# Performance work log

Hardware: AMD Instinct MI355X
Metric: run time of the kernel (lower is better)

## Reference

```python
import jax, jax.numpy as jnp
import numpy as np

HEADS, DIM_HEAD = 8, 96
DIM = HEADS * DIM_HEAD            # 768
DEPTH = 8
MEM_LAYERS = (4, 5)               # layers with KNN-retrieval attention
TOPK = 32                         # num_retrieved_memories
CLIP_LEN, PREFIX_LEN = 10, 10
NEG = -1e9


def layernorm(x, g, b):
    m = x.mean(-1, keepdims=True)
    v = ((x - m) ** 2).mean(-1, keepdims=True)
    return (x - m) * jax.lax.rsqrt(v + 1e-5) * g + b


def attention(x, wq_l, wkv_l, wo_l, mem_k=None, mem_v=None):
    # one-headed key/values (memorizing-transformers style), multi-head queries
    b, n, _ = x.shape
    q = (x @ wq_l).reshape(b, n, HEADS, DIM_HEAD).transpose(0, 2, 1, 3)  # [b,h,n,d]
    q = q * (DIM_HEAD ** -0.5)
    kv = x @ wkv_l                                   # [b,n,2d]
    k, v = kv[..., :DIM_HEAD], kv[..., DIM_HEAD:]    # [b,n,d] each
    sim = jnp.einsum('bhid,bjd->bhij', q, k)         # local scores
    causal = jnp.tril(jnp.ones((n, n), dtype=bool))
    sim = jnp.where(causal, sim, NEG)
    if mem_k is not None:
        # exact inner-product top-k retrieval from per-batch memory bank
        mem_sim = jnp.einsum('bhid,bmd->bhim', q, mem_k)      # [b,h,n,M]
        top_sim, top_idx = jax.lax.top_k(mem_sim, TOPK)       # [b,h,n,K]
        mem_v_sel = jnp.take_along_axis(
            mem_v[:, None, None], top_idx[..., None], axis=3)  # [b,h,n,K,d]
        attn = jax.nn.softmax(jnp.concatenate([top_sim, sim], axis=-1), axis=-1)
        mem_attn, loc_attn = attn[..., :TOPK], attn[..., TOPK:]
        out = (jnp.einsum('bhij,bhijd->bhid', mem_attn, mem_v_sel)
               + jnp.einsum('bhij,bjd->bhid', loc_attn, v))
    else:
        attn = jax.nn.softmax(sim, axis=-1)
        out = jnp.einsum('bhij,bjd->bhid', attn, v)
    out = out.transpose(0, 2, 1, 3).reshape(b, n, DIM)
    return out @ wo_l


def setup_inputs() -> dict:
    key = jax.random.key(0)
    ks = jax.random.split(key, 12)
    s = 0.02
    inp = {
        'x': jax.random.normal(ks[0], (16, 640), jnp.float32),
        'linear_w': jax.random.normal(ks[1], (640, CLIP_LEN * DIM), jnp.float32) * s,
        'linear_b': jnp.zeros((CLIP_LEN * DIM,), jnp.float32),
        'prefix_const': jax.random.normal(ks[2], (PREFIX_LEN, DIM), jnp.float32),
        'ln1_g': jnp.ones((DEPTH, DIM), jnp.float32),
        'ln1_b': jnp.zeros((DEPTH, DIM), jnp.float32),
        'wq': jax.random.normal(ks[3], (DEPTH, DIM, DIM), jnp.float32) * s,
        'wkv': jax.random.normal(ks[4], (DEPTH, DIM, 2 * DIM_HEAD), jnp.float32) * s,
        'wo': jax.random.normal(ks[5], (DEPTH, DIM, DIM), jnp.float32) * s,
        'ln2_g': jnp.ones((DEPTH, DIM), jnp.float32),
        'ln2_b': jnp.zeros((DEPTH, DIM), jnp.float32),
        'w1': jax.random.normal(ks[6], (DEPTH, DIM, 4 * DIM), jnp.float32) * s,
        'b1': jnp.zeros((DEPTH, 4 * DIM), jnp.float32),
        'w2': jax.random.normal(ks[7], (DEPTH, 4 * DIM, DIM), jnp.float32) * s,
        'b2': jnp.zeros((DEPTH, DIM), jnp.float32),
        'lnf_g': jnp.ones((DIM,), jnp.float32),
        'lnf_b': jnp.zeros((DIM,), jnp.float32),
        'mem_k': jax.random.normal(ks[8], (16, 32768, DIM_HEAD), jnp.float32),
        'mem_v': jax.random.normal(ks[9], (16, 32768, DIM_HEAD), jnp.float32),
    }
    return inp


def reference(x, linear_w, linear_b, prefix_const,
              ln1_g, ln1_b, wq, wkv, wo, ln2_g, ln2_b,
              w1, b1, w2, b2, lnf_g, lnf_b, mem_k, mem_v):
    b = x.shape[0]
    # linear projection of clip feature -> clip_length tokens
    h = (x @ linear_w + linear_b).reshape(b, CLIP_LEN, DIM)
    prefix = jnp.broadcast_to(prefix_const[None], (b, PREFIX_LEN, DIM))
    t = jnp.concatenate([h, prefix], axis=1)  # [b, 20, dim]
    for l in range(DEPTH):
        mk, mv = (mem_k, mem_v) if l in MEM_LAYERS else (None, None)
        t = t + attention(layernorm(t, ln1_g[l], ln1_b[l]), wq[l], wkv[l], wo[l], mk, mv)
        hf = layernorm(t, ln2_g[l], ln2_b[l])
        t = t + (jax.nn.gelu(hf @ w1[l] + b1[l]) @ w2[l] + b2[l])
    t = layernorm(t, lnf_g, lnf_b)
    return t[:, CLIP_LEN:]  # [b, prefix_length, dim]
```

## Files before the change

### kernel.cpp

```cpp
#include <hip/hip_runtime.h>
#include <hip/hip_bf16.h>

#define BB 16
#define NSEQ 20
#define HEADS 8
#define DH 96
#define DIM 768
#define FF 3072
#define KMEM 32768
#define NCHUNK 4
#define CHUNK 8192
#define CAP 128

typedef unsigned short u16;
typedef __attribute__((ext_vector_type(8))) short short8v;
typedef __attribute__((ext_vector_type(4))) float f32x4;

__device__ __forceinline__ u16 f2bu(float x) {
    __hip_bfloat16 h = __float2bfloat16(x);
    return *reinterpret_cast<u16*>(&h);
}

__global__ __launch_bounds__(256) void conv_k(const float* __restrict__ src, u16* __restrict__ dst, int n)
{
    int i = blockIdx.x * 256 + threadIdx.x;
    if (i < n) dst[i] = f2bu(src[i]);
}

__device__ __forceinline__ void tconv_tile(const float* __restrict__ src, u16* __restrict__ dst,
                                           int K, int N, int kt, int nt, int tx, int ty)
{
    __shared__ float tile[32][33];
    int k0 = kt * 32, n0 = nt * 32;
#pragma unroll
    for (int i = 0; i < 4; i++)
        tile[ty + 8 * i][tx] = src[(size_t)(k0 + ty + 8 * i) * N + n0 + tx];
    __syncthreads();
#pragma unroll
    for (int i = 0; i < 4; i++)
        dst[(size_t)(n0 + ty + 8 * i) * K + k0 + tx] = f2bu(tile[tx][ty + 8 * i]);
}

__global__ __launch_bounds__(256) void tconv_k(const float* __restrict__ src, u16* __restrict__ dst, int K, int N)
{
    int tilesN = N >> 5;
    tconv_tile(src, dst, K, N, blockIdx.x / tilesN, blockIdx.x % tilesN,
               threadIdx.x & 31, threadIdx.x >> 5);
}

__global__ __launch_bounds__(256) void wconv5L_k(const float* __restrict__ wq, const float* __restrict__ wkv,
    const float* __restrict__ wo, const float* __restrict__ w1, const float* __restrict__ w2,
    u16* __restrict__ wt, size_t wtStride)
{
    int l = blockIdx.y;
    wq += (size_t)l * 589824;
    wkv += (size_t)l * 147456;
    wo += (size_t)l * 589824;
    w1 += (size_t)l * 2359296;
    w2 += (size_t)l * 2359296;
    wt += (size_t)l * wtStride;
    int bx = blockIdx.x;
    int tx = threadIdx.x & 31, ty = threadIdx.x >> 5;
    if (bx < 576)       tconv_tile(wq,  wt + 0,       768, 768,  bx / 24,          bx % 24,          tx, ty);
    else if (bx < 720)  tconv_tile(wkv, wt + 589824,  768, 192,  (bx - 576) / 6,   (bx - 576) % 6,   tx, ty);
    else if (bx < 1296) tconv_tile(wo,  wt + 737280,  768, 768,  (bx - 720) / 24,  (bx - 720) % 24,  tx, ty);
    else if (bx < 3600) tconv_tile(w1,  wt + 1327104, 768, 3072, (bx - 1296) / 96, (bx - 1296) % 96, tx, ty);
    else                tconv_tile(w2,  wt + 3686400, 3072, 768, (bx - 3600) / 24, (bx - 3600) % 24, tx, ty);
}

__device__ __forceinline__ void storeC(float* C, size_t idx, float v) { C[idx] = v; }
__device__ __forceinline__ void storeC(u16* C, size_t idx, float v)   { C[idx] = f2bu(v); }

template <typename CT>
__global__ __launch_bounds__(256) void gemm_bt(const u16* __restrict__ A, const u16* __restrict__ Bt,
    const float* __restrict__ bias, const float* __restrict__ resid, CT* __restrict__ C,
    int M, int N, int K, int lda, int ldc, float scale, int act)
{
    int tid = threadIdx.x;
    int w = tid >> 6, lane = tid & 63;
    int m0 = blockIdx.y * 16;
    int n0 = blockIdx.x * 128 + w * 32;
    int row = lane & 15;
    int kg  = lane >> 4;
    const u16* arow = A + (size_t)(m0 + row) * lda + kg * 8;
    int c0 = n0 + row;
    int c1 = n0 + 16 + row;
    const u16* bt0 = Bt + (size_t)min(c0, N - 1) * K + kg * 8;
    const u16* bt1 = Bt + (size_t)min(c1, N - 1) * K + kg * 8;
    f32x4 acc0 = {0.f, 0.f, 0.f, 0.f};
    f32x4 acc1 = {0.f, 0.f, 0.f, 0.f};
#pragma unroll 4
    for (int k0 = 0; k0 < K; k0 += 32) {
        short8v af = *(const short8v*)(arow + k0);
        short8v b0 = *(const short8v*)(bt0 + k0);
        short8v b1 = *(const short8v*)(bt1 + k0);
        acc0 = __builtin_amdgcn_mfma_f32_16x16x32_bf16(af, b0, acc0, 0, 0, 0);
        acc1 = __builtin_amdgcn_mfma_f32_16x16x32_bf16(af, b1, acc1, 0, 0, 0);
    }
#pragma unroll
    for (int r = 0; r < 4; r++) {
        int rw = m0 + kg * 4 + r;
        if (c0 < N) {
            float v = acc0[r] * scale;
            if (bias) v += bias[c0];
            if (act) {
                float xx = v;
                float tt = 0.7978845608028654f * (xx + 0.044715f * xx * xx * xx);
                v = 0.5f * xx * (1.0f + tanhf(tt));
            }
            if (resid) v += resid[(size_t)rw * ldc + c0];
            storeC(C, (size_t)rw * ldc + c0, v);
        }
        if (c1 < N) {
            float v = acc1[r] * scale;
            if (bias) v += bias[c1];
            if (act) {
                float xx = v;
                float tt = 0.7978845608028654f * (xx + 0.044715f * xx * xx * xx);
                v = 0.5f * xx * (1.0f + tanhf(tt));
            }
            if (resid) v += resid[(size_t)rw * ldc + c1];
            storeC(C, (size_t)rw * ldc + c1, v);
        }
    }
}

__global__ __launch_bounds__(256) void gemm_qkv(const u16* __restrict__ A, const u16* __restrict__ Bt,
    float* __restrict__ qb, float* __restrict__ kvb, float qscale)
{
    const int N = 960, K = DIM;
    int tid = threadIdx.x;
    int w = tid >> 6, lane = tid & 63;
    int m0 = blockIdx.y * 16;
    int n0 = blockIdx.x * 128 + w * 32;
    int row = lane & 15;
    int kg  = lane >> 4;
    const u16* arow = A + (size_t)(m0 + row) * K + kg * 8;
    int c0 = n0 + row;
    int c1 = n0 + 16 + row;
    const u16* bt0 = Bt + (size_t)min(c0, N - 1) * K + kg * 8;
    const u16* bt1 = Bt + (size_t)min(c1, N - 1) * K + kg * 8;
    f32x4 acc0 = {0.f, 0.f, 0.f, 0.f};
    f32x4 acc1 = {0.f, 0.f, 0.f, 0.f};
#pragma unroll 4
    for (int k0 = 0; k0 < K; k0 += 32) {
        short8v af = *(const short8v*)(arow + k0);
        short8v b0 = *(const short8v*)(bt0 + k0);
        short8v b1 = *(const short8v*)(bt1 + k0);
        acc0 = __builtin_amdgcn_mfma_f32_16x16x32_bf16(af, b0, acc0, 0, 0, 0);
        acc1 = __builtin_amdgcn_mfma_f32_16x16x32_bf16(af, b1, acc1, 0, 0, 0);
    }
#pragma unroll
    for (int r = 0; r < 4; r++) {
        int rw = m0 + kg * 4 + r;
        if (c0 < 768)      qb[(size_t)rw * 768 + c0] = acc0[r] * qscale;
        else if (c0 < 960) kvb[(size_t)rw * 192 + (c0 - 768)] = acc0[r];
        if (c1 < 768)      qb[(size_t)rw * 768 + c1] = acc1[r] * qscale;
        else if (c1 < 960) kvb[(size_t)rw * 192 + (c1 - 768)] = acc1[r];
    }
}

__global__ __launch_bounds__(256) void ln_k(const float* __restrict__ x, const float* __restrict__ g,
    const float* __restrict__ bb, u16* __restrict__ y)
{
    int row = blockIdx.x;
    const float* xr = x + (size_t)row * DIM;
    int tid = threadIdx.x;
    float v0 = xr[tid], v1 = xr[tid + 256], v2 = xr[tid + 512];
    __shared__ float red[4];
    float s = v0 + v1 + v2;
    for (int off = 32; off; off >>= 1) s += __shfl_down(s, off);
    if ((tid & 63) == 0) red[tid >> 6] = s;
    __syncthreads();
    float mean = (red[0] + red[1] + red[2] + red[3]) * (1.f / 768.f);
    __syncthreads();
    float d0 = v0 - mean, d1 = v1 - mean, d2 = v2 - mean;
    s = d0 * d0 + d1 * d1 + d2 * d2;
    for (int off = 32; off; off >>= 1) s += __shfl_down(s, off);
    if ((tid & 63) == 0) red[tid >> 6] = s;
    __syncthreads();
    float var = (red[0] + red[1] + red[2] + red[3]) * (1.f / 768.f);
    float rs = rsqrtf(var + 1e-5f);
    u16* yr = y + (size_t)row * DIM;
    yr[tid]       = f2bu(d0 * rs * g[tid]       + bb[tid]);
    yr[tid + 256] = f2bu(d1 * rs * g[tid + 256] + bb[tid + 256]);
    yr[tid + 512] = f2bu(d2 * rs * g[tid + 512] + bb[tid + 512]);
}

__global__ __launch_bounds__(256) void lnf_k(const float* __restrict__ x, const float* __restrict__ g,
    const float* __restrict__ bb, float* __restrict__ out)
{
    int blk = blockIdx.x;
    int b = blk / 10, ii = blk - b * 10;
    int row = b * NSEQ + 10 + ii;
    const float* xr = x + (size_t)row * DIM;
    int tid = threadIdx.x;
    float v0 = xr[tid], v1 = xr[tid + 256], v2 = xr[tid + 512];
    __shared__ float red[4];
    float s = v0 + v1 + v2;
    for (int off = 32; off; off >>= 1) s += __shfl_down(s, off);
    if ((tid & 63) == 0) red[tid >> 6] = s;
    __syncthreads();
    float mean = (red[0] + red[1] + red[2] + red[3]) * (1.f / 768.f);
    __syncthreads();
    float d0 = v0 - mean, d1 = v1 - mean, d2 = v2 - mean;
    s = d0 * d0 + d1 * d1 + d2 * d2;
    for (int off = 32; off; off >>= 1) s += __shfl_down(s, off);
    if ((tid & 63) == 0) red[tid >> 6] = s;
    __syncthreads();
    float var = (red[0] + red[1] + red[2] + red[3]) * (1.f / 768.f);
    float rs = rsqrtf(var + 1e-5f);
    float* orow = out + ((size_t)(b * 10 + ii)) * DIM;
    orow[tid]       = d0 * rs * g[tid]       + bb[tid];
    orow[tid + 256] = d1 * rs * g[tid + 256] + bb[tid + 256];
    orow[tid + 512] = d2 * rs * g[tid + 512] + bb[tid + 512];
}

__global__ __launch_bounds__(256) void prefix_k(const float* __restrict__ p, float* __restrict__ t)
{
    int idx = blockIdx.x * 256 + threadIdx.x;
    if (idx < BB * 7680) {
        int b = idx / 7680;
        int r = idx - b * 7680;
        t[(size_t)b * (NSEQ * DIM) + 7680 + r] = p[r];
    }
}

__device__ __forceinline__ float dot96(const float* __restrict__ a, const float* __restrict__ b)
{
    float s = 0.f;
#pragma unroll
    for (int d4 = 0; d4 < 24; d4++) {
        float4 av = *(const float4*)(a + d4 * 4);
        float4 bv = *(const float4*)(b + d4 * 4);
        s = fmaf(av.x, bv.x, s);
        s = fmaf(av.y, bv.y, s);
        s = fmaf(av.z, bv.z, s);
        s = fmaf(av.w, bv.w, s);
    }
    return s;
}

__global__ __launch_bounds__(256) void lattn_k(const float* __restrict__ q, const float* __restrict__ kv,
    u16* __restrict__ ao)
{
    int b = blockIdx.x, h = blockIdx.y;
    __shared__ float sims[NSEQ][NSEQ];
    __shared__ float probs[NSEQ][NSEQ];
    const float* qb = q + (size_t)b * NSEQ * DIM + h * DH;
    const float* kb = kv + (size_t)b * NSEQ * 192;
    int tid = threadIdx.x;
    for (int p = tid; p < NSEQ * NSEQ; p += 256) {
        int i = p / NSEQ, j = p - i * NSEQ;
        float s;
        if (j > i) s = -1.0e9f;
        else s = dot96(qb + (size_t)i * DIM, kb + j * 192);
        sims[i][j] = s;
    }
    __syncthreads();
    if (tid < NSEQ) {
        int i = tid;
        float m = -1e30f;
        for (int j = 0; j < NSEQ; j++) m = fmaxf(m, sims[i][j]);
        float sum = 0.f;
        for (int j = 0; j < NSEQ; j++) { float e = expf(sims[i][j] - m); probs[i][j] = e; sum += e; }
        float inv = 1.f / sum;
        for (int j = 0; j < NSEQ; j++) probs[i][j] *= inv;
    }
    __syncthreads();
    for (int p = tid; p < NSEQ * DH; p += 256) {
        int i = p / DH, d = p - i * DH;
        float o = 0.f;
        for (int j = 0; j <= i; j++) o = fmaf(probs[i][j], kb[j * 192 + 96 + d], o);
        ao[((size_t)b * NSEQ + i) * DIM + h * DH + d] = f2bu(o);
    }
}

__device__ __forceinline__ bool tk_better(float va, int ia, float vb, int ib) {
    return (va > vb) || (va == vb && ia < ib);
}

__device__ __forceinline__ void lds_fence() {
    asm volatile("s_waitcnt lgkmcnt(0)" ::: "memory");
    __builtin_amdgcn_sched_barrier(0);
}

__device__ void topk32(float* bv, int* bi, int cnt, int lane,
                       float& ov, int& oi, float& thr_out) {
    lds_fence();
    float v0 = (lane < cnt)      ? bv[lane]      : -3.0e38f;
    int   i0 = (lane < cnt)      ? bi[lane]      : 0x7fffffff;
    float v1 = (lane + 64 < cnt) ? bv[lane + 64] : -3.0e38f;
    int   i1 = (lane + 64 < cnt) ? bi[lane + 64] : 0x7fffffff;
    lds_fence();
#pragma unroll
    for (int k = 2; k <= 128; k <<= 1) {
#pragma unroll
        for (int j = 64; j >= 1; j >>= 1) {
            if (j >= k) continue;
            if (j == 64) {
                bool asc = ((lane & k) == 0);
                bool b01 = tk_better(v0, i0, v1, i1);
                if (b01 != asc) { float tv = v0; int ti = i0; v0 = v1; i0 = i1; v1 = tv; i1 = ti; }
            } else {
                {
                    float pv = __shfl_xor(v0, j); int pi = __shfl_xor(i0, j);
                    bool asc = ((lane & k) == 0);
                    bool first = ((lane & j) == 0);
                    bool mb = tk_better(v0, i0, pv, pi);
                    bool keep = first ? (mb == asc) : (mb != asc);
                    if (!keep) { v0 = pv; i0 = pi; }
                }
                {
                    float pv = __shfl_xor(v1, j); int pi = __shfl_xor(i1, j);
                    bool asc = (((lane + 64) & k) == 0);
                    bool first = ((lane & j) == 0);
                    bool mb = tk_better(v1, i1, pv, pi);
                    bool keep = first ? (mb == asc) : (mb != asc);
                    if (!keep) { v1 = pv; i1 = pi; }
                }
            }
        }
    }
    if (lane < 32) { bv[lane] = v0; bi[lane] = i0; }
    lds_fence();
    ov = v0; oi = i0;
    thr_out = __shfl(v0, 31);
}

__device__ __forceinline__ void tk_pass(const float4 kr[6], const float4 qreg[5][6],
    float thrR[5], int cntR[5], float (*bufv)[CAP], int (*bufi)[CAP],
    int r0, int lane, int qt, int key)
{
    float a[5];
#pragma unroll
    for (int rr = 0; rr < 5; rr++) a[rr] = 0.f;
#pragma unroll
    for (int i = 0; i < 6; i++) {
        float4 kv = kr[i];
#pragma unroll
        for (int rr = 0; rr < 5; rr++) {
            float4 qv = qreg[rr][i];
            a[rr] = fmaf(qv.x, kv.x, a[rr]);
            a[rr] = fmaf(qv.y, kv.y, a[rr]);
            a[rr] = fmaf(qv.z, kv.z, a[rr]);
            a[rr] = fmaf(qv.w, kv.w, a[rr]);
        }
    }
#pragma unroll
    for (int rr = 0; rr < 5; rr++) {
        a[rr] += __shfl_xor(a[rr], 1);
        a[rr] += __shfl_xor(a[rr], 2);
    }
#pragma unroll
    for (int rr = 0; rr < 5; rr++) {
        bool cand = (qt == 0) && (a[rr] >= thrR[rr]);
        unsigned long long mask = __ballot(cand);
        int n = __popcll(mask);
        if (n) {
            int r = r0 + rr;
            if (cntR[rr] + n > CAP) {
                float dv; int di;
                topk32(&bufv[r][0], &bufi[r][0], cntR[rr], lane, dv, di, thrR[rr]);
                cntR[rr] = 32;
            }
            int pos = cntR[rr] + __popcll(mask & ((1ull << lane) - 1ull));
            if (cand) { bufv[r][pos] = a[rr]; bufi[r][pos] = key; }
            cntR[rr] += n;
        }
    }
}

__global__ __launch_bounds__(256) __attribute__((amdgpu_waves_per_eu(2, 2)))
void memtopk_k(const float* __restrict__ q, const float* __restrict__ memk,
    float* __restrict__ tkv, int* __restrict__ tki)
{
    __shared__ float bufv[NSEQ][CAP];
    __shared__ int   bufi[NSEQ][CAP];
    int c = blockIdx.x, h = blockIdx.y, b = blockIdx.z;
    int tid = threadIdx.x;
    int lane = tid & 63;
    int w = tid >> 6;
    int r0 = w * 5;
    int qt = lane & 3;
    int kk = lane >> 2;

    float4 qreg[5][6];
#pragma unroll
    for (int rr = 0; rr < 5; rr++) {
        const float4* qrow = (const float4*)(q + ((size_t)(b * NSEQ + r0 + rr)) * DIM + h * DH + qt * 24);
#pragma unroll
        for (int i = 0; i < 6; i++) qreg[rr][i] = qrow[i];
    }

    float thrR[5]; int cntR[5];
#pragma unroll
    for (int rr = 0; rr < 5; rr++) { thrR[rr] = -3.0e38f; cntR[rr] = 0; }

    const float* kbase = memk + (size_t)b * KMEM * DH;
    int k0 = c * CHUNK;

    float4 kA[12], kB[12];
#pragma unroll
    for (int s = 0; s < 2; s++) {
        const float4* kp = (const float4*)(kbase + (size_t)(k0 + s * 16 + kk) * DH + qt * 24);
#pragma unroll
        for (int i = 0; i < 6; i++) kA[s * 6 + i] = kp[i];
    }
    for (int p = 0; p < CHUNK / 16; p += 4) {
        int key0 = k0 + p * 16 + kk;
#pragma unroll
        for (int s = 0; s < 2; s++) {
            const float4* kp = (const float4*)(kbase + (size_t)(key0 + (32 + s * 16)) * DH + qt * 24);
#pragma unroll
            for (int i = 0; i < 6; i++) kB[s * 6 + i] = kp[i];
        }
        tk_pass(kA + 0, qreg, thrR, cntR, bufv, bufi, r0, lane, qt, key0);
        tk_pass(kA + 6, qreg, thrR, cntR, bufv, bufi, r0, lane, qt, key0 + 16);
        if (p + 4 < CHUNK / 16) {
#pragma unroll
            for (int s = 0; s < 2; s++) {
                const float4* kp = (const float4*)(kbase + (size_t)(key0 + (64 + s * 16)) * DH + qt * 24);
#pragma unroll
                for (int i = 0; i < 6; i++) kA[s * 6 + i] = kp[i];
            }
        }
        tk_pass(kB + 0, qreg, thrR, cntR, bufv, bufi, r0, lane, qt, key0 + 32);
        tk_pass(kB + 6, qreg, thrR, cntR, bufv, bufi, r0, lane, qt, key0 + 48);
    }
#pragma unroll
    for (int rr = 0; rr < 5; rr++) {
        int r = r0 + rr;
        float ov; int oi; float dthr;
        topk32(&bufv[r][0], &bufi[r][0], cntR[rr], lane, ov, oi, dthr);
        if (lane < 32) {
            size_t base = ((((size_t)b * HEADS + h) * NSEQ + r) * NCHUNK + c) * 32;
            tkv[base + lane] = ov;
            tki[base + lane] = oi;
        }
    }
}

__global__ __launch_bounds__(64) void memattn_k(const float* __restrict__ q, const float* __restrict__ kv,
    const float* __restrict__ memv, const float* __restrict__ tkv, const int* __restrict__ tki,
    u16* __restrict__ ao)
{
    int i = blockIdx.x, h = blockIdx.y, b = blockIdx.z;
    __shared__ float cv[NCHUNK * 32];
    __shared__ int   ci[NCHUNK * 32];
    __shared__ float selv[32];
    __shared__ int   seli[32];
    __shared__ float ls[NSEQ];
    __shared__ float probs[52];
    int tid = threadIdx.x;
    size_t base = (((size_t)b * HEADS + h) * NSEQ + i) * (NCHUNK * 32);
#pragma unroll
    for (int s = 0; s < NCHUNK * 32 / 64; s++) {
        cv[tid + 64 * s] = tkv[base + tid + 64 * s];
        ci[tid + 64 * s] = tki[base + tid + 64 * s];
    }
    const float* qr = q + ((size_t)b * NSEQ + i) * DIM + h * DH;
    const float* kvb = kv + (size_t)b * NSEQ * 192;
    if (tid <= i) {
        float s = dot96(qr, kvb + tid * 192);
        ls[tid] = s;
    }
    __syncthreads();
    for (int r = 0; r < 32; r++) {
        float bv = -3.0e38f; int bidx = 0x7fffffff; int bs = 0;
#pragma unroll
        for (int s = 0; s < NCHUNK * 32 / 64; s++) {
            float v = cv[tid + 64 * s]; int ix = ci[tid + 64 * s];
            if (tk_better(v, ix, bv, bidx)) { bv = v; bidx = ix; bs = tid + 64 * s; }
        }
        for (int off = 32; off; off >>= 1) {
            float ovv = __shfl_down(bv, off);
            int oii = __shfl_down(bidx, off);
            int oss = __shfl_down(bs, off);
            if (tk_better(ovv, oii, bv, bidx)) { bv = ovv; bidx = oii; bs = oss; }
        }
        if (tid == 0) { selv[r] = bv; seli[r] = bidx; cv[bs] = -3.0e38f; }
        __syncthreads();
    }
    if (tid == 0) {
        float m = -1e30f;
        for (int r = 0; r < 32; r++) m = fmaxf(m, selv[r]);
        for (int j = 0; j <= i; j++) m = fmaxf(m, ls[j]);
        float sum = 0.f;
        for (int r = 0; r < 32; r++) { float e = expf(selv[r] - m); probs[r] = e; sum += e; }
        for (int j = 0; j <= i; j++) { float e = expf(ls[j] - m); probs[32 + j] = e; sum += e; }
        float inv = 1.f / sum;
        for (int r = 0; r < 32 + i + 1; r++) probs[r] *= inv;
    }
    __syncthreads();
    const float* mvb = memv + (size_t)b * KMEM * DH;
    for (int d = tid; d < DH; d += 64) {
        float o = 0.f;
        for (int r = 0; r < 32; r++) o = fmaf(probs[r], mvb[(size_t)seli[r] * DH + d], o);
        for (int j = 0; j <= i; j++) o = fmaf(probs[32 + j], kvb[j * 192 + 96 + d], o);
        ao[((size_t)b * NSEQ + i) * DIM + h * DH + d] = f2bu(o);
    }
}

extern "C" void kernel_launch(void* const* d_in, const int* in_sizes, int n_in,
                              void* d_out, int out_size, void* d_ws, size_t ws_size,
                              hipStream_t stream) {
    const float* x            = (const float*)d_in[0];
    const float* linear_w     = (const float*)d_in[1];
    const float* linear_b     = (const float*)d_in[2];
    const float* prefix_const = (const float*)d_in[3];
    const float* ln1_g        = (const float*)d_in[4];
    const float* ln1_b        = (const float*)d_in[5];
    const float* wq           = (const float*)d_in[6];
    const float* wkv          = (const float*)d_in[7];
    const float* wo           = (const float*)d_in[8];
    const float* ln2_g        = (const float*)d_in[9];
    const float* ln2_b        = (const float*)d_in[10];
    const float* w1           = (const float*)d_in[11];
    const float* b1           = (const float*)d_in[12];
    const float* w2           = (const float*)d_in[13];
    const float* b2           = (const float*)d_in[14];
    const float* lnf_g        = (const float*)d_in[15];
    const float* lnf_b        = (const float*)d_in[16];
    const float* mem_k        = (const float*)d_in[17];
    const float* mem_v        = (const float*)d_in[18];

    float* ws = (float*)d_ws;
    float* t    = ws;
    u16*   yb   = (u16*)(ws + 245760);
    float* qb   = ws + 491520;
    float* kvb  = ws + 737280;
    u16*   aob  = (u16*)(ws + 798720);
    u16*   h1b  = (u16*)(ws + 1044480);
    float* tkv  = ws + 2027520;
    int*   tki  = (int*)(ws + 2355200);
    u16*   wt   = (u16*)(ws + 2682880);
    float* out  = (float*)d_out;

    const size_t LAYER_WT = 6045696;
    const int all8 = (ws_size >= (size_t)(2682880 + 8 * 3022848 + 2560) * 4) ? 1 : 0;
    u16* xb = (u16*)(ws + (all8 ? (2682880 + 8 * 3022848) : (2682880 + 3022848)));

    const float qscale = 0.10206207261596577f;
    const size_t WOT = 737280, W1T = 1327104, W2T = 3686400;

    conv_k<<<40, 256, 0, stream>>>(x, xb, 16 * 640);
    tconv_k<<<4800, 256, 0, stream>>>(linear_w, wt, 640, 7680);
    gemm_bt<float><<<dim3(60, 1), 256, 0, stream>>>(xb, wt, linear_b, nullptr, t,
                                                    16, 7680, 640, 640, 15360, 1.f, 0);
    prefix_k<<<dim3(480), 256, 0, stream>>>(prefix_const, t);

    if (all8)
        wconv5L_k<<<dim3(5904, 8), 256, 0, stream>>>(wq, wkv, wo, w1, w2, wt, LAYER_WT);

    for (int l = 0; l < 8; l++) {
        u16* wtl = wt + (all8 ? (size_t)l * LAYER_WT : 0);
        if (!all8)
            wconv5L_k<<<dim3(5904, 1), 256, 0, stream>>>(wq + (size_t)l * 589824, wkv + (size_t)l * 147456,
                                                         wo + (size_t)l * 589824, w1 + (size_t)l * 2359296,
                                                         w2 + (size_t)l * 2359296, wtl, 0);
        ln_k<<<320, 256, 0, stream>>>(t, ln1_g + (size_t)l * DIM, ln1_b + (size_t)l * DIM, yb);
        gemm_qkv<<<dim3(8, 20), 256, 0, stream>>>(yb, wtl, qb, kvb, qscale);
        if (l == 4 || l == 5) {
            memtopk_k<<<dim3(NCHUNK, HEADS, BB), 256, 0, stream>>>(qb, mem_k, tkv, tki);
            memattn_k<<<dim3(NSEQ, HEADS, BB), 64, 0, stream>>>(qb, kvb, mem_v, tkv, tki, aob);
        } else {
            lattn_k<<<dim3(BB, HEADS), 256, 0, stream>>>(qb, kvb, aob);
        }
        gemm_bt<float><<<dim3(6, 20), 256, 0, stream>>>(aob, wtl + WOT, nullptr, t, t,
                                                        320, 768, 768, 768, 768, 1.f, 0);
        ln_k<<<320, 256, 0, stream>>>(t, ln2_g + (size_t)l * DIM, ln2_b + (size_t)l * DIM, yb);
        gemm_bt<u16><<<dim3(24, 20), 256, 0, stream>>>(yb, wtl + W1T, b1 + (size_t)l * FF, nullptr, h1b,
                                                       320, 3072, 768, 768, 3072, 1.f, 1);
        gemm_bt<float><<<dim3(6, 20), 256, 0, stream>>>(h1b, wtl + W2T, b2 + (size_t)l * DIM, t, t,
                                                        320, 768, 3072, 3072, 768, 1.f, 0);
    }
    lnf_k<<<160, 256, 0, stream>>>(t, lnf_g, lnf_b, out);
}
```

Measured before the change: 2.078 ms.

## Fuse layernorm into QKV and FFN-up GEMMs, batch ballots in top-k scan

Removes the standalone layernorm kernels. The QKV and W1 GEMMs now each normalize their 16-row A tile into shared memory before running the MFMA loop, which saves 16 launches and the bf16 round trip through global memory. The cost is that every column block recomputes the layernorm for its rows (8x or 24x redundant work). The memory top-k scan also gathers all five row ballots first and skips the insertion path when none are set, to cut divergent branching in the hot loop.

```diff
diff --git a/kernel.cpp b/kernel.cpp
--- a/kernel.cpp
+++ b/kernel.cpp
@@ -11,6 +11,7 @@
 #define NCHUNK 4
 #define CHUNK 8192
 #define CAP 128
+#define ALDS 776
 
 typedef unsigned short u16;
 typedef __attribute__((ext_vector_type(8))) short short8v;
@@ -125,17 +126,63 @@
     }
 }
 
-__global__ __launch_bounds__(256) void gemm_qkv(const u16* __restrict__ A, const u16* __restrict__ Bt,
+__device__ __forceinline__ void ln_stage(const float* __restrict__ t, const float* __restrict__ g,
+    const float* __restrict__ bln, int m0, int tid, u16* __restrict__ As)
+{
+    int lane = tid & 63, w = tid >> 6;
+    int rl = w * 4 + (lane >> 4);
+    int sl = lane & 15;
+    const float4* tr = (const float4*)(t + (size_t)(m0 + rl) * DIM);
+    float4 xv[12];
+    float sum = 0.f;
+#pragma unroll
+    for (int i = 0; i < 12; i++) {
+        xv[i] = tr[i * 16 + sl];
+        sum += xv[i].x + xv[i].y + xv[i].z + xv[i].w;
+    }
+    sum += __shfl_xor(sum, 1); sum += __shfl_xor(sum, 2);
+    sum += __shfl_xor(sum, 4); sum += __shfl_xor(sum, 8);
+    float mean = sum * (1.f / 768.f);
+    float vs = 0.f;
+#pragma unroll
+    for (int i = 0; i < 12; i++) {
+        float dx = xv[i].x - mean, dy = xv[i].y - mean;
+        float dz = xv[i].z - mean, dw2 = xv[i].w - mean;
+        vs += dx * dx + dy * dy + dz * dz + dw2 * dw2;
+    }
+    vs += __shfl_xor(vs, 1); vs += __shfl_xor(vs, 2);
+    vs += __shfl_xor(vs, 4); vs += __shfl_xor(vs, 8);
+    float rs = rsqrtf(vs * (1.f / 768.f) + 1e-5f);
+    u16* arow = As + (size_t)rl * ALDS;
+#pragma unroll
+    for (int i = 0; i < 12; i++) {
+        int col = i * 64 + sl * 4;
+        float4 gv = *(const float4*)(g + col);
+        float4 bv = *(const float4*)(bln + col);
+        ushort4 ov;
+        ov.x = f2bu((xv[i].x - mean) * rs * gv.x + bv.x);
+        ov.y = f2bu((xv[i].y - mean) * rs * gv.y + bv.y);
+        ov.z = f2bu((xv[i].z - mean) * rs * gv.z + bv.z);
+        ov.w = f2bu((xv[i].w - mean) * rs * gv.w + bv.w);
+        *(ushort4*)(arow + col) = ov;
+    }
+}
+
+__global__ __launch_bounds__(256) void gemm_ln_qkv(const float* __restrict__ t,
+    const float* __restrict__ g, const float* __restrict__ bln, const u16* __restrict__ Bt,
     float* __restrict__ qb, float* __restrict__ kvb, float qscale)
 {
+    __shared__ u16 As[16 * ALDS];
     const int N = 960, K = DIM;
     int tid = threadIdx.x;
+    int m0 = blockIdx.y * 16;
+    ln_stage(t, g, bln, m0, tid, As);
+    __syncthreads();
     int w = tid >> 6, lane = tid & 63;
-    int m0 = blockIdx.y * 16;
     int n0 = blockIdx.x * 128 + w * 32;
     int row = lane & 15;
     int kg  = lane >> 4;
-    const u16* arow = A + (size_t)(m0 + row) * K + kg * 8;
+    const u16* arow = As + (size_t)row * ALDS + kg * 8;
     int c0 = n0 + row;
     int c1 = n0 + 16 + row;
     const u16* bt0 = Bt + (size_t)min(c0, N - 1) * K + kg * 8;
@@ -160,31 +207,51 @@
     }
 }
 
-__global__ __launch_bounds__(256) void ln_k(const float* __restrict__ x, const float* __restrict__ g,
-    const float* __restrict__ bb, u16* __restrict__ y)
-{
-    int row = blockIdx.x;
-    const float* xr = x + (size_t)row * DIM;
+__global__ __launch_bounds__(256) void gemm_ln_w1(const float* __restrict__ t,
+    const float* __restrict__ g, const float* __restrict__ bln, const u16* __restrict__ Bt,
+    const float* __restrict__ bias, u16* __restrict__ C)
+{
+    __shared__ u16 As[16 * ALDS];
+    const int N = FF, K = DIM;
     int tid = threadIdx.x;
-    float v0 = xr[tid], v1 = xr[tid + 256], v2 = xr[tid + 512];
-    __shared__ float red[4];
-    float s = v0 + v1 + v2;
-    for (int off = 32; off; off >>= 1) s += __shfl_down(s, off);
-    if ((tid & 63) == 0) red[tid >> 6] = s;
-    __syncthreads();
-    float mean = (red[0] + red[1] + red[2] + red[3]) * (1.f / 768.f);
-    __syncthreads();
-    float d0 = v0 - mean, d1 = v1 - mean, d2 = v2 - mean;
-    s = d0 * d0 + d1 * d1 + d2 * d2;
-    for (int off = 32; off; off >>= 1) s += __shfl_down(s, off);
-    if ((tid & 63) == 0) red[tid >> 6] = s;
-    __syncthreads();
-    float var = (red[0] + red[1] + red[2] + red[3]) * (1.f / 768.f);
-    float rs = rsqrtf(var + 1e-5f);
-    u16* yr = y + (size_t)row * DIM;
-    yr[tid]       = f2bu(d0 * rs * g[tid]       + bb[tid]);
-    yr[tid + 256] = f2bu(d1 * rs * g[tid + 256] + bb[tid + 256]);
-    yr[tid + 512] = f2bu(d2 * rs * g[tid + 512] + bb[tid + 512]);
+    int m0 = blockIdx.y * 16;
+    ln_stage(t, g, bln, m0, tid, As);
+    __syncthreads();
+    int w = tid >> 6, lane = tid & 63;
+    int n0 = blockIdx.x * 128 + w * 32;
+    int row = lane & 15;
+    int kg  = lane >> 4;
+    const u16* arow = As + (size_t)row * ALDS + kg * 8;
+    int c0 = n0 + row;
+    int c1 = n0 + 16 + row;
+    const u16* bt0 = Bt + (size_t)c0 * K + kg * 8;
+    const u16* bt1 = Bt + (size_t)c1 * K + kg * 8;
+    f32x4 acc0 = {0.f, 0.f, 0.f, 0.f};
+    f32x4 acc1 = {0.f, 0.f, 0.f, 0.f};
+#pragma unroll 4
+    for (int k0 = 0; k0 < K; k0 += 32) {
+        short8v af = *(const short8v*)(arow + k0);
+        short8v b0 = *(const short8v*)(bt0 + k0);
+        short8v b1 = *(const short8v*)(bt1 + k0);
+        acc0 = __builtin_amdgcn_mfma_f32_16x16x32_bf16(af, b0, acc0, 0, 0, 0);
+        acc1 = __builtin_amdgcn_mfma_f32_16x16x32_bf16(af, b1, acc1, 0, 0, 0);
+    }
+#pragma unroll
+    for (int r = 0; r < 4; r++) {
+        int rw = m0 + kg * 4 + r;
+        {
+            float v = acc0[r] + bias[c0];
+            float tt = 0.7978845608028654f * (v + 0.044715f * v * v * v);
+            v = 0.5f * v * (1.0f + tanhf(tt));
+            C[(size_t)rw * FF + c0] = f2bu(v);
+        }
+        {
+            float v = acc1[r] + bias[c1];
+            float tt = 0.7978845608028654f * (v + 0.044715f * v * v * v);
+            v = 0.5f * v * (1.0f + tanhf(tt));
+            C[(size_t)rw * FF + c1] = f2bu(v);
+        }
+    }
 }
 
 __global__ __launch_bounds__(256) void lnf_k(const float* __restrict__ x, const float* __restrict__ g,
@@ -352,21 +419,27 @@
         a[rr] += __shfl_xor(a[rr], 1);
         a[rr] += __shfl_xor(a[rr], 2);
     }
+    unsigned long long m[5];
 #pragma unroll
     for (int rr = 0; rr < 5; rr++) {
         bool cand = (qt == 0) && (a[rr] >= thrR[rr]);
-        unsigned long long mask = __ballot(cand);
-        int n = __popcll(mask);
-        if (n) {
-            int r = r0 + rr;
-            if (cntR[rr] + n > CAP) {
-                float dv; int di;
-                topk32(&bufv[r][0], &bufi[r][0], cntR[rr], lane, dv, di, thrR[rr]);
-                cntR[rr] = 32;
+        m[rr] = __ballot(cand);
+    }
+    if (m[0] | m[1] | m[2] | m[3] | m[4]) {
+#pragma unroll
+        for (int rr = 0; rr < 5; rr++) {
+            if (m[rr]) {
+                int n = __popcll(m[rr]);
+                int r = r0 + rr;
+                if (cntR[rr] + n > CAP) {
+                    float dv; int di;
+                    topk32(&bufv[r][0], &bufi[r][0], cntR[rr], lane, dv, di, thrR[rr]);
+                    cntR[rr] = 32;
+                }
+                int pos = cntR[rr] + __popcll(m[rr] & ((1ull << lane) - 1ull));
+                if ((m[rr] >> lane) & 1ull) { bufv[r][pos] = a[rr]; bufi[r][pos] = key; }
+                cntR[rr] += n;
             }
-            int pos = cntR[rr] + __popcll(mask & ((1ull << lane) - 1ull));
-            if (cand) { bufv[r][pos] = a[rr]; bufi[r][pos] = key; }
-            cntR[rr] += n;
         }
     }
 }
@@ -536,6 +609,7 @@
     int*   tki  = (int*)(ws + 2355200);
     u16*   wt   = (u16*)(ws + 2682880);
     float* out  = (float*)d_out;
+    (void)yb;
 
     const size_t LAYER_WT = 6045696;
     const int all8 = (ws_size >= (size_t)(2682880 + 8 * 3022848 + 2560) * 4) ? 1 : 0;
@@ -559,8 +633,8 @@
             wconv5L_k<<<dim3(5904, 1), 256, 0, stream>>>(wq + (size_t)l * 589824, wkv + (size_t)l * 147456,
                                                          wo + (size_t)l * 589824, w1 + (size_t)l * 2359296,
                                                          w2 + (size_t)l * 2359296, wtl, 0);
-        ln_k<<<320, 256, 0, stream>>>(t, ln1_g + (size_t)l * DIM, ln1_b + (size_t)l * DIM, yb);
-        gemm_qkv<<<dim3(8, 20), 256, 0, stream>>>(yb, wtl, qb, kvb, qscale);
+        gemm_ln_qkv<<<dim3(8, 20), 256, 0, stream>>>(t, ln1_g + (size_t)l * DIM, ln1_b + (size_t)l * DIM,
+                                                     wtl, qb, kvb, qscale);
         if (l == 4 || l == 5) {
             memtopk_k<<<dim3(NCHUNK, HEADS, BB), 256, 0, stream>>>(qb, mem_k, tkv, tki);
             memattn_k<<<dim3(NSEQ, HEADS, BB), 64, 0, stream>>>(qb, kvb, mem_v, tkv, tki, aob);
@@ -569,9 +643,8 @@
         }
         gemm_bt<float><<<dim3(6, 20), 256, 0, stream>>>(aob, wtl + WOT, nullptr, t, t,
                                                         320, 768, 768, 768, 768, 1.f, 0);
-        ln_k<<<320, 256, 0, stream>>>(t, ln2_g + (size_t)l * DIM, ln2_b + (size_t)l * DIM, yb);
-        gemm_bt<u16><<<dim3(24, 20), 256, 0, stream>>>(yb, wtl + W1T, b1 + (size_t)l * FF, nullptr, h1b,
-                                                       320, 3072, 768, 768, 3072, 1.f, 1);
+        gemm_ln_w1<<<dim3(24, 20), 256, 0, stream>>>(t, ln2_g + (size_t)l * DIM, ln2_b + (size_t)l * DIM,
+                                                     wtl + W1T, b1 + (size_t)l * FF, h1b);
         gemm_bt<float><<<dim3(6, 20), 256, 0, stream>>>(h1b, wtl + W2T, b2 + (size_t)l * DIM, t, t,
                                                         320, 768, 3072, 3072, 768, 1.f, 0);
     }
```

New measurement: 1.988 ms. 1.05x faster.
